# Performance work log

Hardware: AMD Instinct MI355X
Metric: run time of the kernel (lower is better)

Reference implementation:

```python
import jax, jax.numpy as jnp
import numpy as np

COMMIT = 0.5  # commitment from Discriminator init


def _sn(w):
    """Spectral norm, 1 power iteration from a deterministic start vector."""
    W = w.reshape(w.shape[0], -1)
    u = jnp.ones((W.shape[0],), w.dtype) / jnp.sqrt(jnp.asarray(W.shape[0], w.dtype))
    v = W.T @ u
    v = jax.lax.stop_gradient(v / (jnp.linalg.norm(v) + 1e-8))
    u2 = W @ v
    u2 = jax.lax.stop_gradient(u2 / (jnp.linalg.norm(u2) + 1e-8))
    sigma = u2 @ (W @ v)
    return w / sigma


def _conv(h, w, b, pad):
    y = jax.lax.conv_general_dilated(h, _sn(w), (1, 1), [(pad, pad), (pad, pad)],
                                     dimension_numbers=("NCHW", "OIHW", "NCHW"))
    return y + b[None, :, None, None]


def _pool(h):  # AvgPool2d(2)
    B, C, H, W = h.shape
    return h.reshape(B, C, H // 2, 2, W // 2, 2).mean(axis=(3, 5))


def _dblock(h, w1, b1, w2, b2, wsc, bsc, preact, down):
    y = jax.nn.relu(h) if preact else h
    y = _conv(y, w1, b1, 1)
    y = _conv(jax.nn.relu(y), w2, b2, 1)
    if down:
        y = _pool(y)
    sc = h
    if preact:
        if wsc is not None:
            sc = _conv(sc, wsc, bsc, 0)
        if down:
            sc = _pool(sc)
    else:
        if down:
            sc = _pool(sc)
        if wsc is not None:
            sc = _conv(sc, wsc, bsc, 0)
    return y + sc


def _quantize(h, embed):
    """VQ step (eval mode, no EMA). h: [B,C,H,W], embed: [C,K]."""
    B, C, H, W = h.shape
    xp = jnp.transpose(h, (0, 2, 3, 1))            # [B,H,W,C]
    flat = xp.reshape(-1, C)                       # [N,C]
    dist = (jnp.sum(flat ** 2, 1, keepdims=True)
            - 2.0 * flat @ embed
            + jnp.sum(embed ** 2, 0, keepdims=True))  # [N,K]
    ind = jnp.argmin(dist, axis=1)                 # [N]
    q = embed.T[ind].reshape(xp.shape)             # gather codebook rows
    diff = COMMIT * jnp.mean((jax.lax.stop_gradient(q) - xp) ** 2, axis=(1, 2, 3)).reshape(B, 1)
    q_st = xp + jax.lax.stop_gradient(q - xp)      # straight-through (unused downstream, as in source)
    K = embed.shape[1]
    probs = jnp.zeros((K,), flat.dtype).at[ind].add(1.0) / flat.shape[0]
    ppl = jnp.exp(-jnp.sum(probs * jnp.log(probs + 1e-10)))
    return jnp.transpose(q_st, (0, 3, 1, 2)), diff, ppl


def setup_inputs() -> dict:
    key = jax.random.key(0)
    ks = iter(jax.random.split(key, 40))
    d = {}
    d["x"] = jax.random.normal(next(ks), (64, 3, 32, 32), jnp.float32)
    d["y"] = jax.random.randint(next(ks), (64,), 0, 100)
    def w(shape):
        return 0.02 * jax.random.normal(next(ks), shape, jnp.float32)
    # block 0: 3->256, downsample, learnable sc
    d["b0_w1"] = w((256, 3, 3, 3));   d["b0_b1"] = jnp.zeros((256,), jnp.float32)
    d["b0_w2"] = w((256, 256, 3, 3)); d["b0_b2"] = jnp.zeros((256,), jnp.float32)
    d["b0_wsc"] = w((256, 3, 1, 1)); d["b0_bsc"] = jnp.zeros((256,), jnp.float32)
    # block 1: 256->256, downsample, learnable sc
    d["b1_w1"] = w((256, 256, 3, 3)); d["b1_b1"] = jnp.zeros((256,), jnp.float32)
    d["b1_w2"] = w((256, 256, 3, 3)); d["b1_b2"] = jnp.zeros((256,), jnp.float32)
    d["b1_wsc"] = w((256, 256, 1, 1)); d["b1_bsc"] = jnp.zeros((256,), jnp.float32)
    # blocks 2,3: 256->256, no downsample, identity sc
    d["b2_w1"] = w((256, 256, 3, 3)); d["b2_b1"] = jnp.zeros((256,), jnp.float32)
    d["b2_w2"] = w((256, 256, 3, 3)); d["b2_b2"] = jnp.zeros((256,), jnp.float32)
    d["b3_w1"] = w((256, 256, 3, 3)); d["b3_b1"] = jnp.zeros((256,), jnp.float32)
    d["b3_w2"] = w((256, 256, 3, 3)); d["b3_b2"] = jnp.zeros((256,), jnp.float32)
    # VQ codebooks: torch.randn(dim, n_embed)
    for i in range(4):
        d[f"cb{i}"] = jax.random.normal(next(ks), (256, 1024), jnp.float32)
    d["lin_w"] = w((1, 256)); d["lin_b"] = jnp.zeros((1,), jnp.float32)
    d["emb_w"] = w((100, 256))
    return d


def reference(x, y, b0_w1, b0_b1, b0_w2, b0_b2, b0_wsc, b0_bsc,
              b1_w1, b1_b1, b1_w2, b1_b2, b1_wsc, b1_bsc,
              b2_w1, b2_b1, b2_w2, b2_b2, b3_w1, b3_b1, b3_w2, b3_b2,
              cb0, cb1, cb2, cb3, lin_w, lin_b, emb_w):
    h = _dblock(x, b0_w1, b0_b1, b0_w2, b0_b2, b0_wsc, b0_bsc, preact=False, down=True)
    _, d0, _ = _quantize(h, cb0)   # quantized output discarded, as in source
    h = _dblock(h, b1_w1, b1_b1, b1_w2, b1_b2, b1_wsc, b1_bsc, preact=True, down=True)
    _, d1, _ = _quantize(h, cb1)
    h = _dblock(h, b2_w1, b2_b1, b2_w2, b2_b2, None, None, preact=True, down=False)
    _, d2, _ = _quantize(h, cb2)
    h = _dblock(h, b3_w1, b3_b1, b3_w2, b3_b2, None, None, preact=True, down=False)
    _, d3, ppl = _quantize(h, cb3)
    quant_loss = d0 + d1 + d2 + d3                 # [B,1]
    hf = jnp.sum(jax.nn.relu(h), axis=(2, 3))      # [B,256]
    out = hf @ _sn(lin_w).T + lin_b                # [B,1]
    out = out + jnp.sum(_sn(emb_w)[y] * hf, axis=1, keepdims=True)
    return (out, quant_loss, ppl)
```

## Files before the change

kernel.cpp:

```cpp
#include <hip/hip_runtime.h>
#include <math.h>

typedef __attribute__((ext_vector_type(8))) short s8v;
typedef __attribute__((ext_vector_type(4))) float f4v;

__device__ inline ushort f2bf(float x) {
    unsigned u = __float_as_uint(x);
    unsigned r = (u + 0x7FFFu + ((u >> 16) & 1u)) >> 16;
    return (ushort)r;
}
__device__ inline float bf2f(ushort h) { return __uint_as_float(((unsigned)h) << 16); }
__device__ inline float sig_of(double n2) { return (float)(n2 / (sqrt(n2) + 1e-8)); }

#define DEV __global__ __launch_bounds__(256)

struct SnMeta { const float* w[12]; int O[12]; int M[12]; };
struct SnRMap { short mat[85]; short row0[85]; };

DEV void snv2_kernel(SnMeta a, SnRMap mp, double* __restrict__ vbufraw) {
    int b = blockIdx.x;
    int id = mp.mat[b];
    int r0 = mp.row0[b];
    int O = a.O[id], M = a.M[id];
    int rend = min(r0 + 32, O);
    const float* W = a.w[id];
    for (int m = threadIdx.x; m < M; m += 256) {
        double s = 0.0;
        for (int o = r0; o < rend; ++o) s += (double)W[(size_t)o * M + m];
        atomicAdd(vbufraw + id * 2304 + m, s);
    }
}

DEV void snn_kernel(SnMeta a, const double* __restrict__ vbufraw, double* __restrict__ vnorm2) {
    int id = blockIdx.x;
    int M = a.M[id];
    double u0 = 1.0 / sqrt((double)a.O[id]);
    __shared__ double red[256];
    double ps = 0.0;
    for (int m = threadIdx.x; m < M; m += 256) { double v = vbufraw[id * 2304 + m] * u0; ps += v * v; }
    red[threadIdx.x] = ps; __syncthreads();
    for (int st = 128; st > 0; st >>= 1) { if (threadIdx.x < st) red[threadIdx.x] += red[threadIdx.x + st]; __syncthreads(); }
    if (threadIdx.x == 0) vnorm2[id] = red[0];
}

DEV void snu_kernel(SnMeta a, const double* __restrict__ vbufraw,
                    const double* __restrict__ vnorm2, double* __restrict__ unorm2) {
    int wv = blockIdx.x * 4 + (threadIdx.x >> 6);
    int lane = threadIdx.x & 63;
    const int cumR[13] = {0, 256, 512, 768, 1024, 1280, 1536, 1792, 2048, 2304, 2560, 2561, 2661};
    if (wv >= 2661) return;
    int id = 0;
    for (int i = 0; i < 12; ++i) if (wv >= cumR[i]) id = i;
    int o = wv - cumR[id];
    int M = a.M[id];
    double u0 = 1.0 / sqrt((double)a.O[id]);
    const float* Wr = a.w[id] + (size_t)o * M;
    const double* vb = vbufraw + id * 2304;
    double s = 0.0;
    for (int m = lane; m < M; m += 64) s += (double)Wr[m] * vb[m];
    for (int off = 32; off > 0; off >>= 1) s += __shfl_down(s, off, 64);
    if (lane == 0) {
        double s1 = 1.0 / (sqrt(vnorm2[id]) + 1e-8);
        double u = s * u0 * s1;
        atomicAdd(unorm2 + id, u * u);
    }
}

struct PrepArgs {
    const float* w[8]; int C[8]; int sigidx[8]; int outoff[8]; int nel[8];
    const float* cb[4];
};

DEV void prep_all_kernel(PrepArgs a, const double* __restrict__ unorm2,
                         ushort* __restrict__ wp, ushort* __restrict__ ep,
                         double* __restrict__ en64) {
    int blk = blockIdx.x;
    if (blk < 1824) {
        int gid = blk * 256 + threadIdx.x;
        int L = 0, cum = 0;
        for (int i = 0; i < 8; ++i) { int n9 = a.nel[i] / 9; if (gid >= cum && gid < cum + n9) { L = i; break; } cum += a.nel[i] / 9; }
        if (gid >= cum + a.nel[L] / 9) return;
        int e9 = gid - cum;
        if (L == 0) {
            int oc = e9 >> 5, k = e9 & 31;
            float inv = 1.f / sig_of(unorm2[0]);
            float v = 0.f;
            if (k < 27) v = a.w[0][((size_t)(oc * 3 + (k % 3))) * 9 + (k / 3)] * inv;
            ushort h = f2bf(v);
            ushort l = f2bf(v - bf2f(h));
            wp[oc * 32 + k] = h;
            wp[8192 + oc * 32 + k] = l;
            return;
        }
        int C = a.C[L];
        int NICC = (C + 31) >> 5;
        int icl = e9 & 31;
        int oc = (e9 >> 5) & 255;
        int icc = e9 >> 13;
        int ic = icc * 32 + icl;
        float inv = 1.f / sig_of(unorm2[a.sigidx[L]]);
        const float* wr = (ic < C) ? (a.w[L] + ((size_t)oc * C + ic) * 9) : nullptr;
        int nel = a.nel[L];
        int base = a.outoff[L] + icc * 8192 + oc * 32 + icl;
        #pragma unroll
        for (int tap = 0; tap < 9; ++tap) {
            float v = wr ? wr[tap] * inv : 0.f;
            ushort h = f2bf(v);
            ushort l = f2bf(v - bf2f(h));
            int o = base + tap * NICC * 8192;
            wp[o] = h;
            wp[o + nel] = l;
        }
    } else if (blk < 1824 + 4096) {
        int gid = (blk - 1824) * 256 + threadIdx.x;
        int layer = gid >> 18;
        int e = gid & 262143;
        int c5 = e & 31, k = (e >> 5) & 1023, icc = e >> 15;
        float v = a.cb[layer][(size_t)(icc * 32 + c5) * 1024 + k];
        ushort h = f2bf(v);
        ushort l = f2bf(v - bf2f(h));
        size_t o = (size_t)layer * 524288 + ((size_t)icc * 1024 + k) * 64 + c5;
        ep[o] = h; ep[o + 32] = l;
    } else {
        int b2 = blk - 1824 - 4096;
        int cc = b2 & 7, layer = b2 >> 3;
        const float* cb = a.cb[layer];
        int t = threadIdx.x;
        double d[4] = {};
        for (int c = cc * 32; c < cc * 32 + 32; ++c) {
            #pragma unroll
            for (int j = 0; j < 4; ++j) {
                double v = (double)cb[(size_t)c * 1024 + t + j * 256];
                d[j] += v * v;
            }
        }
        #pragma unroll
        for (int j = 0; j < 4; ++j) atomicAdd(en64 + layer * 1024 + t + j * 256, d[j]);
    }
}

DEV void enfin_kernel(const double* __restrict__ en64, float* __restrict__ en) {
    int gid = blockIdx.x * 256 + threadIdx.x;
    en[gid] = (float)en64[gid];
}

__global__ __launch_bounds__(256) void conv01k_kernel(
        const float* __restrict__ x, const ushort* __restrict__ wp0,
        const float* __restrict__ bias, ushort* __restrict__ outs) {
    __shared__ float sX[3][10][10];
    __shared__ ushort sI[64][72];
    int t = threadIdx.x, wid = t >> 6, lane = t & 63, quad = lane >> 4, l15 = lane & 15;
    int n = blockIdx.z;
    int tIdx = blockIdx.x;
    int th0 = (tIdx >> 2) * 8, tw0 = (tIdx & 3) * 8;
    for (int i = t; i < 300; i += 256) {
        int ch = i / 100, r = i - (i / 100) * 100;
        int yy = r / 10, xx = r - (r / 10) * 10;
        int gy = th0 - 1 + yy, gx = tw0 - 1 + xx;
        float v = 0.f;
        if (gy >= 0 && gy < 32 && gx >= 0 && gx < 32) v = x[(((size_t)n * 3 + ch) * 32 + gy) * 32 + gx];
        sX[ch][yy][xx] = v;
    }
    __syncthreads();
    for (int i = t; i < 2048; i += 256) {
        int px = i >> 5, k = i & 31;
        float v = 0.f;
        if (k < 27) {
            int tap = k / 3, ch = k - tap * 3;
            int ty = tap / 3, tx = tap - ty * 3;
            v = sX[ch][(px >> 3) + ty][(px & 7) + tx];
        }
        ushort hv = f2bf(v);
        sI[px][k] = hv;
        sI[px][32 + k] = f2bf(v - bf2f(hv));
    }
    __syncthreads();
    int ocb = wid * 64;
    f4v acc[4][4];
    #pragma unroll
    for (int mt = 0; mt < 4; ++mt)
        #pragma unroll
        for (int nt = 0; nt < 4; ++nt) acc[mt][nt] = (f4v){0.f, 0.f, 0.f, 0.f};
    s8v ah[4], al[4], bh[4], bl[4];
    #pragma unroll
    for (int mt = 0; mt < 4; ++mt) {
        ah[mt] = *(const s8v*)&sI[mt * 16 + l15][quad * 8];
        al[mt] = *(const s8v*)&sI[mt * 16 + l15][32 + quad * 8];
    }
    #pragma unroll
    for (int nt = 0; nt < 4; ++nt) {
        int oc = ocb + nt * 16 + l15;
        bh[nt] = *(const s8v*)(wp0 + oc * 32 + quad * 8);
        bl[nt] = *(const s8v*)(wp0 + 8192 + oc * 32 + quad * 8);
    }
    #pragma unroll
    for (int mt = 0; mt < 4; ++mt)
        #pragma unroll
        for (int nt = 0; nt < 4; ++nt) {
            acc[mt][nt] = __builtin_amdgcn_mfma_f32_16x16x32_bf16(al[mt], bh[nt], acc[mt][nt], 0, 0, 0);
            acc[mt][nt] = __builtin_amdgcn_mfma_f32_16x16x32_bf16(ah[mt], bl[nt], acc[mt][nt], 0, 0, 0);
            acc[mt][nt] = __builtin_amdgcn_mfma_f32_16x16x32_bf16(ah[mt], bh[nt], acc[mt][nt], 0, 0, 0);
        }
    #pragma unroll
    for (int nt = 0; nt < 4; ++nt) {
        int oc = ocb + nt * 16 + l15;
        float bv = bias[oc];
        int iccg = oc >> 5, ocw = oc & 31;
        #pragma unroll
        for (int mt = 0; mt < 4; ++mt) {
            #pragma unroll
            for (int r = 0; r < 4; ++r) {
                int px = mt * 16 + quad * 4 + r;
                int y = th0 + (px >> 3), xx = tw0 + (px & 7);
                float v = fmaxf(acc[mt][nt][r] + bv, 0.f);
                ushort h = f2bf(v);
                size_t ob = ((((size_t)n * 32 + y) * 32 + xx) * 8 + iccg) * 64;
                outs[ob + ocw] = h;
                outs[ob + 32 + ocw] = f2bf(v - bf2f(h));
            }
        }
    }
}

template<int PX>
DEV void vq2_kernel(const float* __restrict__ h, const float* __restrict__ cb,
                    const ushort* __restrict__ ep, const float* __restrict__ en,
                    float* __restrict__ dacc, int* __restrict__ hist,
                    ushort* __restrict__ hs, int HW) {
    const int MT = PX / 16;
    const int SUBS = 256 / PX;
    __shared__ ushort sA[8 * PX * 66];
    __shared__ unsigned long long sKey[PX][65];
    __shared__ int sKst[PX];
    __shared__ float sPart[PX][SUBS];
    __shared__ double sSum[PX];
    int t = threadIdx.x, wid = t >> 6, lane = t & 63, quad = lane >> 4, l15 = lane & 15;
    int pix0 = blockIdx.x * PX, n = pix0 / HW, s0 = pix0 % HW;
    const float* hb = h + (size_t)n * 256 * HW + s0;

    for (int i = t; i < 256 * PX; i += 256) {
        int c = i / PX, p = i % PX;
        float v = hb[(size_t)c * HW + p];
        ushort hv = f2bf(v), lv = f2bf(v - bf2f(hv));
        int a = (c >> 5) * (PX * 66) + p * 66 + (c & 31);
        sA[a] = hv; sA[a + 32] = lv;
    }
    __syncthreads();

    if (hs) {
        for (int i = t; i < PX * 32; i += 256) {
            int p = i >> 5; int rem = i & 31; int icc = rem >> 2, q = rem & 3;
            int aoff = icc * (PX * 66) + p * 66 + q * 8;
            s8v hv = *(const s8v*)&sA[aoff];
            s8v lv = *(const s8v*)&sA[aoff + 32];
            #pragma unroll
            for (int j = 0; j < 8; ++j) {
                float f = bf2f((ushort)hv[j]) + bf2f((ushort)lv[j]);
                if (f <= 0.f) { hv[j] = 0; lv[j] = 0; }
            }
            size_t ob = (((size_t)n * HW + s0 + p) * 8 + icc) * 64 + q * 8;
            *(s8v*)(hs + ob) = hv;
            *(s8v*)(hs + ob + 32) = lv;
        }
    }

    unsigned long long best[MT][4];
    #pragma unroll
    for (int mt = 0; mt < MT; ++mt)
        #pragma unroll
        for (int r = 0; r < 4; ++r) best[mt][r] = ~0ull;

    for (int kp = 0; kp < 2; ++kp) {
        f4v acc[MT][8];
        #pragma unroll
        for (int mt = 0; mt < MT; ++mt)
            #pragma unroll
            for (int nt = 0; nt < 8; ++nt) acc[mt][nt] = (f4v){0.f, 0.f, 0.f, 0.f};
        for (int icc = 0; icc < 8; ++icc) {
            #pragma unroll
            for (int ntc = 0; ntc < 2; ++ntc) {
                s8v eh[4], el[4];
                #pragma unroll
                for (int j = 0; j < 4; ++j) {
                    int k = wid * 256 + kp * 128 + (ntc * 4 + j) * 16 + l15;
                    const ushort* q = ep + ((size_t)icc * 1024 + k) * 64 + quad * 8;
                    eh[j] = *(const s8v*)q; el[j] = *(const s8v*)(q + 32);
                }
                #pragma unroll
                for (int mt = 0; mt < MT; ++mt) {
                    int a = icc * (PX * 66) + (mt * 16 + l15) * 66 + quad * 8;
                    s8v ah = *(const s8v*)&sA[a], al = *(const s8v*)&sA[a + 32];
                    #pragma unroll
                    for (int j = 0; j < 4; ++j) {
                        int nt = ntc * 4 + j;
                        acc[mt][nt] = __builtin_amdgcn_mfma_f32_16x16x32_bf16(al, eh[j], acc[mt][nt], 0, 0, 0);
                        acc[mt][nt] = __builtin_amdgcn_mfma_f32_16x16x32_bf16(ah, el[j], acc[mt][nt], 0, 0, 0);
                        acc[mt][nt] = __builtin_amdgcn_mfma_f32_16x16x32_bf16(ah, eh[j], acc[mt][nt], 0, 0, 0);
                    }
                }
            }
        }
        #pragma unroll
        for (int mt = 0; mt < MT; ++mt)
            #pragma unroll
            for (int nt = 0; nt < 8; ++nt) {
                int k = wid * 256 + kp * 128 + nt * 16 + l15;
                float ev = en[k];
                #pragma unroll
                for (int r = 0; r < 4; ++r) {
                    float s = ev - 2.f * acc[mt][nt][r];
                    unsigned ub = __float_as_uint(s);
                    ub = ((int)ub < 0) ? ~ub : (ub | 0x80000000u);
                    unsigned long long key = ((unsigned long long)ub << 32) | (unsigned)k;
                    if (key < best[mt][r]) best[mt][r] = key;
                }
            }
    }
    #pragma unroll
    for (int mt = 0; mt < MT; ++mt)
        #pragma unroll
        for (int r = 0; r < 4; ++r) {
            int p = mt * 16 + quad * 4 + r;
            sKey[p][wid * 16 + l15] = best[mt][r];
        }
    __syncthreads();
    if (t < PX) {
        unsigned long long m = ~0ull;
        for (int j = 0; j < 64; ++j) { unsigned long long v = sKey[t][j]; if (v < m) m = v; }
        sKst[t] = (int)(unsigned)(m & 0xFFFFFFFFu);
    }
    __syncthreads();
    {
        int p = t % PX, sub = t / PX;
        int ks = sKst[p];
        const float* ec = cb + ks;
        float d = 0.f;
        for (int c = sub * PX; c < sub * PX + PX; ++c) {
            float xv = hb[(size_t)c * HW + p];
            float evv = ec[(size_t)c * 1024];
            float df = xv - evv;
            d += df * df;
        }
        sPart[p][sub] = d;
    }
    __syncthreads();
    if (t < PX) {
        float s = 0.f;
        for (int j = 0; j < SUBS; ++j) s += sPart[t][j];
        sSum[t] = (double)s;
        if (hist) atomicAdd(hist + sKst[t], 1);
    }
    __syncthreads();
    if (t == 0) {
        double s = 0.0;
        for (int i = 0; i < PX; ++i) s += sSum[i];
        atomicAdd(dacc + n, (float)s);
    }
}

template<int ST, int NW, int NTW, int NICC, bool RELU, bool POOL, bool RES, bool INS, bool OUTS, bool SC0>
__global__ __launch_bounds__(NW * 64) void conv_mfma(
        const float* __restrict__ in, const ushort* __restrict__ ins,
        const ushort* __restrict__ wp, const float* __restrict__ bias,
        const float* __restrict__ res, float* __restrict__ out,
        ushort* __restrict__ outs, int C, int H,
        const float* __restrict__ scw, const float* __restrict__ scb,
        const double* __restrict__ un2) {
    const int MT = ST * 4;
    const int PLANE = NICC * 73728;
    const int SASZ = ST * 100 * 72;
    const int NITER = (ST * 100 * 8 + NW * 64 - 1) / (NW * 64);
    __shared__ ushort sA[(INS ? 2 : 1) * SASZ];
    __shared__ float sSC[3][16];
    int t = threadIdx.x;
    int wid = t >> 6, lane = t & 63, quad = lane >> 4, l15 = lane & 15;
    int n = blockIdx.z;
    int ocb = blockIdx.y * (NW * NTW * 16) + wid * (NTW * 16);
    int tpr = H >> 3;
    int tIdx0 = blockIdx.x * ST;

    int abase[MT];
    #pragma unroll
    for (int mt = 0; mt < MT; ++mt) {
        int m64 = (mt & 3) * 16 + l15;
        abase[mt] = (((mt >> 2) * 100 + (m64 >> 3) * 10 + (m64 & 7)) * 72) + quad * 8;
    }

    unsigned gofs[INS ? NITER : 1];
    s8v pref[INS ? NITER : 1];
    if (INS) {
        #pragma unroll
        for (int it = 0; it < NITER; ++it) {
            int i = t + it * NW * 64;
            gofs[it] = 0xFFFFFFFFu;
            if (i < ST * 100 * 8) {
                int pg = i >> 3, part = i & 7;
                int tile = pg / 100, pos = pg - tile * 100;
                int tIdx = tIdx0 + tile;
                int th0 = (tIdx / tpr) * 8, tw0 = (tIdx % tpr) * 8;
                int gy = th0 - 1 + pos / 10, gx = tw0 - 1 + (pos % 10);
                if (gy >= 0 && gy < H && gx >= 0 && gx < H)
                    gofs[it] = (unsigned)((((n * H + gy) * H + gx) * 8) * 64 + part * 8);
            }
        }
        #pragma unroll
        for (int it = 0; it < NITER; ++it)
            pref[it] = (gofs[it] != 0xFFFFFFFFu) ? *(const s8v*)(ins + gofs[it])
                                                 : (s8v){0, 0, 0, 0, 0, 0, 0, 0};
        #pragma unroll
        for (int it = 0; it < NITER; ++it) {
            int i = t + it * NW * 64;
            if (i < ST * 100 * 8) *(s8v*)(&sA[(i >> 3) * 72 + (i & 7) * 8]) = pref[it];
        }
        if (NICC > 1) {
            #pragma unroll
            for (int it = 0; it < NITER; ++it)
                pref[it] = (gofs[it] != 0xFFFFFFFFu) ? *(const s8v*)(ins + gofs[it] + 64)
                                                     : (s8v){0, 0, 0, 0, 0, 0, 0, 0};
        }
        __syncthreads();
    }

    f4v acc[MT][NTW];
    #pragma unroll
    for (int mt = 0; mt < MT; ++mt)
        #pragma unroll
        for (int nt = 0; nt < NTW; ++nt)
            acc[mt][nt] = (f4v){0.f, 0.f, 0.f, 0.f};

    for (int icc = 0; icc < NICC; ++icc) {
        int bufbase = INS ? (icc & 1) * SASZ : 0;
        if (INS) {
            if (icc + 1 < NICC) {
                int nb = ((icc + 1) & 1) * SASZ;
                #pragma unroll
                for (int it = 0; it < NITER; ++it) {
                    int i = t + it * NW * 64;
                    if (i < ST * 100 * 8) *(s8v*)(&sA[nb + (i >> 3) * 72 + (i & 7) * 8]) = pref[it];
                }
                if (icc + 2 < NICC) {
                    #pragma unroll
                    for (int it = 0; it < NITER; ++it)
                        pref[it] = (gofs[it] != 0xFFFFFFFFu) ? *(const s8v*)(ins + gofs[it] + (unsigned)(icc + 2) * 64)
                                                             : (s8v){0, 0, 0, 0, 0, 0, 0, 0};
                }
            }
        } else {
            __syncthreads();
            for (int i = t; i < ST * 100 * 32; i += NW * 64) {
                int ic = i / (ST * 100);
                int rr = i - ic * (ST * 100);
                int tile = rr / 100, pos = rr - (rr / 100) * 100;
                int tIdx = tIdx0 + tile;
                int th0 = (tIdx / tpr) * 8, tw0 = (tIdx % tpr) * 8;
                int gy = th0 - 1 + pos / 10, gx = tw0 - 1 + (pos % 10);
                int gic = icc * 32 + ic;
                ushort hv = 0, lv = 0;
                if (gic < C && gy >= 0 && gy < H && gx >= 0 && gx < H) {
                    float v = in[(((size_t)n * C + gic) * H + gy) * H + gx];
                    if (RELU) v = fmaxf(v, 0.f);
                    hv = f2bf(v);
                    lv = f2bf(v - bf2f(hv));
                }
                int si = (tile * 100 + pos) * 72 + ic;
                sA[si] = hv; sA[si + 32] = lv;
            }
            __syncthreads();
        }

        s8v bh[2][NTW], bl[2][NTW];
        {
            size_t wb = (size_t)icc * 8192;
            #pragma unroll
            for (int nt = 0; nt < NTW; ++nt) {
                size_t wo = wb + (size_t)(ocb + nt * 16 + l15) * 32 + quad * 8;
                bh[0][nt] = *(const s8v*)(wp + wo);
                bl[0][nt] = *(const s8v*)(wp + PLANE + wo);
            }
        }
        #pragma unroll
        for (int tap = 0; tap < 9; ++tap) {
            int cb = tap & 1;
            if (tap < 8) {
                size_t wb = (size_t)((tap + 1) * NICC + icc) * 8192;
                #pragma unroll
                for (int nt = 0; nt < NTW; ++nt) {
                    size_t wo = wb + (size_t)(ocb + nt * 16 + l15) * 32 + quad * 8;
                    bh[cb ^ 1][nt] = *(const s8v*)(wp + wo);
                    bl[cb ^ 1][nt] = *(const s8v*)(wp + PLANE + wo);
                }
            }
            int toff = ((tap / 3) * 10 + (tap % 3)) * 72;
            #pragma unroll
            for (int mt = 0; mt < MT; ++mt) {
                s8v ah = *(const s8v*)(&sA[bufbase + abase[mt] + toff]);
                s8v al = *(const s8v*)(&sA[bufbase + abase[mt] + toff + 32]);
                #pragma unroll
                for (int nt = 0; nt < NTW; ++nt) {
                    acc[mt][nt] = __builtin_amdgcn_mfma_f32_16x16x32_bf16(al, bh[cb][nt], acc[mt][nt], 0, 0, 0);
                    acc[mt][nt] = __builtin_amdgcn_mfma_f32_16x16x32_bf16(ah, bl[cb][nt], acc[mt][nt], 0, 0, 0);
                    acc[mt][nt] = __builtin_amdgcn_mfma_f32_16x16x32_bf16(ah, bh[cb][nt], acc[mt][nt], 0, 0, 0);
                }
            }
        }
        if (INS && icc + 1 < NICC) __syncthreads();
    }

    if (SC0) {
        __syncthreads();
        if (t < 48) {
            int ic = t >> 4, p = t & 15;
            int py = p >> 2, px = p & 3;
            int th0 = (tIdx0 / tpr) * 8, tw0 = (tIdx0 % tpr) * 8;
            const float* xb = in + (((size_t)(n * 3 + ic)) * 32 + th0 + 2 * py) * 32 + tw0 + 2 * px;
            sSC[ic][p] = 0.25f * (xb[0] + xb[1] + xb[32] + xb[33]);
        }
        __syncthreads();
    }

    #pragma unroll
    for (int nt = 0; nt < NTW; ++nt) {
        int oc = ocb + nt * 16 + l15;
        float bv = bias[oc];
        #pragma unroll
        for (int mt = 0; mt < MT; ++mt) {
            int tIdx = tIdx0 + (mt >> 2);
            int th0 = (tIdx / tpr) * 8, tw0 = (tIdx % tpr) * 8;
            if (POOL) {
                float s01 = acc[mt][nt][0] + acc[mt][nt][1];
                float s23 = acc[mt][nt][2] + acc[mt][nt][3];
                float o01 = s01 + __shfl_down(s01, 32, 64);
                float o23 = s23 + __shfl_down(s23, 32, 64);
                if (quad < 2) {
                    int Ho = H >> 1;
                    int oy = (th0 >> 1) + (mt & 3);
                    int ox = (tw0 >> 1) + quad * 2;
                    size_t ob = ((size_t)(n * 256 + oc) * Ho + oy) * Ho;
                    float v0 = 0.25f * o01 + bv;
                    float v1 = 0.25f * o23 + bv;
                    if (SC0) {
                        int p0 = (mt & 3) * 4 + quad * 2;
                        float scale = 1.f / sig_of(un2[2]);
                        float sa0 = scb[oc], sa1 = scb[oc];
                        #pragma unroll
                        for (int ic = 0; ic < 3; ++ic) {
                            float wv = scw[oc * 3 + ic] * scale;
                            sa0 += sSC[ic][p0] * wv;
                            sa1 += sSC[ic][p0 + 1] * wv;
                        }
                        v0 += sa0;
                        v1 += sa1;
                    }
                    out[ob + ox] = v0;
                    out[ob + ox + 1] = v1;
                }
            } else if (OUTS) {
                int iccg = oc >> 5, ocw = oc & 31;
                #pragma unroll
                for (int r = 0; r < 4; ++r) {
                    int p16 = quad * 4 + r;
                    int y = th0 + (mt & 3) * 2 + (p16 >> 3);
                    int x = tw0 + (p16 & 7);
                    float v = fmaxf(acc[mt][nt][r] + bv, 0.f);
                    ushort h = f2bf(v);
                    size_t ob = ((((size_t)n * H + y) * H + x) * 8 + iccg) * 64;
                    outs[ob + ocw] = h;
                    outs[ob + 32 + ocw] = f2bf(v - bf2f(h));
                }
            } else {
                #pragma unroll
                for (int r = 0; r < 4; ++r) {
                    int p16 = quad * 4 + r;
                    int y = th0 + (mt & 3) * 2 + (p16 >> 3);
                    int x = tw0 + (p16 & 7);
                    size_t oi = (((size_t)(n * 256 + oc)) * H + y) * H + x;
                    float v = acc[mt][nt][r] + bv;
                    if (RES) v += res[oi];
                    out[oi] = v;
                }
            }
        }
    }
}

DEV void sc1_kernel(const float* __restrict__ h1, const float* __restrict__ wsc,
                    const float* __restrict__ bsc, const double* __restrict__ unorm2,
                    float* __restrict__ h2) {
    __shared__ float sP[64][64];
    __shared__ float sWs[64][65];
    int t = threadIdx.x;
    int n = blockIdx.x, ocb = blockIdx.y * 64;
    int ocg = t & 15, pgr = t >> 4;
    float scale = 1.f / sig_of(unorm2[5]);
    float acc[4][4] = {};
    for (int c0 = 0; c0 < 256; c0 += 64) {
        __syncthreads();
        for (int i = t; i < 4096; i += 256) {
            int ic = i >> 6, p = i & 63;
            int oh = p >> 3, ow = p & 7;
            const float* hb = h1 + (((size_t)(n * 256 + c0 + ic)) * 16 + oh * 2) * 16 + ow * 2;
            sP[ic][p] = 0.25f * (hb[0] + hb[1] + hb[16] + hb[17]);
            int oc = i >> 6, ic2 = i & 63;
            sWs[oc][ic2] = wsc[(size_t)(ocb + oc) * 256 + c0 + ic2] * scale;
        }
        __syncthreads();
        for (int ic = 0; ic < 64; ++ic) {
            float pv[4];
            #pragma unroll
            for (int q = 0; q < 4; ++q) pv[q] = sP[ic][pgr * 4 + q];
            #pragma unroll
            for (int j = 0; j < 4; ++j) {
                float wv = sWs[ocg + 16 * j][ic];
                #pragma unroll
                for (int q = 0; q < 4; ++q) acc[j][q] += wv * pv[q];
            }
        }
    }
    #pragma unroll
    for (int j = 0; j < 4; ++j) {
        int oc = ocb + ocg + 16 * j;
        float bv = bsc[oc];
        #pragma unroll
        for (int q = 0; q < 4; ++q) {
            size_t oi = ((size_t)(n * 256 + oc)) * 64 + pgr * 4 + q;
            h2[oi] += acc[j][q] + bv;
        }
    }
}

DEV void headppl_kernel(const float* __restrict__ h4, const float* __restrict__ lin_w,
                        const float* __restrict__ lin_b, const float* __restrict__ emb_w,
                        const int* __restrict__ y, const double* __restrict__ unorm2,
                        const float* __restrict__ dacc, const int* __restrict__ hist,
                        float* __restrict__ out) {
    __shared__ double r1[256], r2[256];
    int b = blockIdx.x, t = threadIdx.x;
    const float* hb = h4 + ((size_t)b * 256 + t) * 64;
    float s = 0.f;
    #pragma unroll 4
    for (int i = 0; i < 64; ++i) s += fmaxf(hb[i], 0.f);
    int yb = y[b];
    r1[t] = (double)s * (double)lin_w[t];
    r2[t] = (double)s * (double)emb_w[(size_t)yb * 256 + t];
    __syncthreads();
    for (int st = 128; st > 0; st >>= 1) { if (t < st) { r1[t] += r1[t + st]; r2[t] += r2[t + st]; } __syncthreads(); }
    if (t == 0) {
        out[b] = (float)(r1[0] / (double)sig_of(unorm2[10]) + (double)lin_b[0] + r2[0] / (double)sig_of(unorm2[11]));
        out[64 + b] = (float)(0.5 * ((double)dacc[b] * (1.0 / 65536.0)
                              + ((double)dacc[64 + b] + (double)dacc[128 + b] + (double)dacc[192 + b]) * (1.0 / 16384.0)));
    }
    if (b == 0) {
        __syncthreads();
        double ps = 0.0;
        for (int k = t; k < 1024; k += 256) {
            double p = (double)hist[k] * (1.0 / 4096.0);
            ps += p * log(p + 1e-10);
        }
        r1[t] = ps; __syncthreads();
        for (int st = 128; st > 0; st >>= 1) { if (t < st) r1[t] += r1[t + st]; __syncthreads(); }
        if (t == 0) out[128] = (float)exp(-r1[0]);
    }
}

extern "C" void kernel_launch(void* const* d_in, const int* in_sizes, int n_in,
                              void* d_out, int out_size, void* d_ws, size_t ws_size,
                              hipStream_t stream) {
    (void)in_sizes; (void)n_in; (void)out_size; (void)ws_size;
    const float* x      = (const float*)d_in[0];
    const int*   y      = (const int*)  d_in[1];
    const float* b0_w1  = (const float*)d_in[2];
    const float* b0_b1  = (const float*)d_in[3];
    const float* b0_w2  = (const float*)d_in[4];
    const float* b0_b2  = (const float*)d_in[5];
    const float* b0_wsc = (const float*)d_in[6];
    const float* b0_bsc = (const float*)d_in[7];
    const float* b1_w1  = (const float*)d_in[8];
    const float* b1_b1  = (const float*)d_in[9];
    const float* b1_w2  = (const float*)d_in[10];
    const float* b1_b2  = (const float*)d_in[11];
    const float* b1_wsc = (const float*)d_in[12];
    const float* b1_bsc = (const float*)d_in[13];
    const float* b2_w1  = (const float*)d_in[14];
    const float* b2_b1  = (const float*)d_in[15];
    const float* b2_w2  = (const float*)d_in[16];
    const float* b2_b2  = (const float*)d_in[17];
    const float* b3_w1  = (const float*)d_in[18];
    const float* b3_b1  = (const float*)d_in[19];
    const float* b3_w2  = (const float*)d_in[20];
    const float* b3_b2  = (const float*)d_in[21];
    const float* cb0    = (const float*)d_in[22];
    const float* cb1    = (const float*)d_in[23];
    const float* cb2    = (const float*)d_in[24];
    const float* cb3    = (const float*)d_in[25];
    const float* lin_w  = (const float*)d_in[26];
    const float* lin_b  = (const float*)d_in[27];
    const float* emb_w  = (const float*)d_in[28];
    float* out = (float*)d_out;

    float* wsf  = (float*)d_ws;
    float* dacc = wsf + 16;
    double* vnorm2 = (double*)(wsf + 512);
    double* unorm2 = (double*)(wsf + 544);
    int*   hist = (int*)(wsf + 1296);
    double* en64 = (double*)(wsf + 2560);
    float* en   = wsf + 10752;
    ushort* Aus  = (ushort*)(wsf + 65536);
    ushort* tbus = (ushort*)(wsf + 65536);
    ushort* t2us = (ushort*)(wsf + 4259840);
    ushort* h1s  = (ushort*)(wsf + 5308416);
    ushort* h2s  = (ushort*)(wsf + 9502720);
    ushort* h3s  = (ushort*)(wsf + 10551296);
    float* h1 = wsf + 16842752;
    float* h2 = h1 + 4194304;
    float* h3 = h2 + 1048576;
    float* h4 = h3 + 1048576;
    ushort* wp = (ushort*)(wsf + 24182784);
    double* vbufraw = (double*)(wsf + 28385280);
    ushort* ep = (ushort*)(wsf + 28440576);

    hipMemsetAsync(wsf, 0, 10752 * sizeof(float), stream);
    hipMemsetAsync(vbufraw, 0, 27648 * sizeof(double), stream);

    SnMeta sm;
    const float* sw[12] = {b0_w1, b0_w2, b0_wsc, b1_w1, b1_w2, b1_wsc,
                           b2_w1, b2_w2, b3_w1, b3_w2, lin_w, emb_w};
    int sO[12] = {256, 256, 256, 256, 256, 256, 256, 256, 256, 256, 1, 100};
    int sM[12] = {27, 2304, 3, 2304, 2304, 256, 2304, 2304, 2304, 2304, 256, 256};
    for (int i = 0; i < 12; ++i) { sm.w[i] = sw[i]; sm.O[i] = sO[i]; sm.M[i] = sM[i]; }
    SnRMap rp;
    {
        int bi = 0;
        for (int i = 0; i < 12; ++i) {
            int nb = (sO[i] + 31) / 32;
            for (int j = 0; j < nb; ++j) { rp.mat[bi] = (short)i; rp.row0[bi] = (short)(j * 32); ++bi; }
        }
    }
    snv2_kernel<<<85, 256, 0, stream>>>(sm, rp, vbufraw);
    snn_kernel<<<12, 256, 0, stream>>>(sm, vbufraw, vnorm2);
    snu_kernel<<<666, 256, 0, stream>>>(sm, vbufraw, vnorm2, unorm2);

    PrepArgs pa;
    const float* pw[8] = {b0_w1, b0_w2, b1_w1, b1_w2, b2_w1, b2_w2, b3_w1, b3_w2};
    int pC[8]   = {3, 256, 256, 256, 256, 256, 256, 256};
    int pS[8]   = {0, 1, 3, 4, 6, 7, 8, 9};
    int pOff[8] = {0, 147456, 1327104, 2506752, 3686400, 4866048, 6045696, 7225344};
    int pN[8]   = {73728, 589824, 589824, 589824, 589824, 589824, 589824, 589824};
    for (int i = 0; i < 8; ++i) { pa.w[i] = pw[i]; pa.C[i] = pC[i]; pa.sigidx[i] = pS[i]; pa.outoff[i] = pOff[i]; pa.nel[i] = pN[i]; }
    pa.cb[0] = cb0; pa.cb[1] = cb1; pa.cb[2] = cb2; pa.cb[3] = cb3;
    prep_all_kernel<<<5952, 256, 0, stream>>>(pa, unorm2, wp, ep, en64);
    enfin_kernel<<<16, 256, 0, stream>>>(en64, en);

    conv01k_kernel<<<dim3(16, 1, 64), 256, 0, stream>>>(x, wp, b0_b1, Aus);
    conv_mfma<1, 4, 2, 8, false, true, false, true, false, true><<<dim3(16, 2, 64), 256, 0, stream>>>(
        x, Aus, wp + 147456, b0_b2, nullptr, h1, nullptr, 256, 32, b0_wsc, b0_bsc, unorm2);
    vq2_kernel<32><<<512, 256, 0, stream>>>(h1, cb0, ep + 0, en + 0, dacc + 0, nullptr, h1s, 256);

    conv_mfma<1, 4, 1, 8, false, false, false, true, true, false><<<dim3(4, 4, 64), 256, 0, stream>>>(
        nullptr, h1s, wp + 1327104, b1_b1, nullptr, nullptr, tbus, 256, 16, nullptr, nullptr, nullptr);
    conv_mfma<1, 4, 1, 8, false, true, false, true, false, false><<<dim3(4, 4, 64), 256, 0, stream>>>(
        nullptr, tbus, wp + 2506752, b1_b2, nullptr, h2, nullptr, 256, 16, nullptr, nullptr, nullptr);
    sc1_kernel<<<dim3(64, 4), 256, 0, stream>>>(h1, b1_wsc, b1_bsc, unorm2, h2);
    vq2_kernel<16><<<256, 256, 0, stream>>>(h2, cb1, ep + 524288, en + 1024, dacc + 64, nullptr, h2s, 64);

    conv_mfma<1, 2, 1, 8, false, false, false, true, true, false><<<dim3(1, 8, 64), 128, 0, stream>>>(
        nullptr, h2s, wp + 3686400, b2_b1, nullptr, nullptr, t2us, 256, 8, nullptr, nullptr, nullptr);
    conv_mfma<1, 2, 1, 8, false, false, true, true, false, false><<<dim3(1, 8, 64), 128, 0, stream>>>(
        nullptr, t2us, wp + 4866048, b2_b2, h2, h3, nullptr, 256, 8, nullptr, nullptr, nullptr);
    vq2_kernel<16><<<256, 256, 0, stream>>>(h3, cb2, ep + 1048576, en + 2048, dacc + 128, nullptr, h3s, 64);

    conv_mfma<1, 2, 1, 8, false, false, false, true, true, false><<<dim3(1, 8, 64), 128, 0, stream>>>(
        nullptr, h3s, wp + 6045696, b3_b1, nullptr, nullptr, t2us, 256, 8, nullptr, nullptr, nullptr);
    conv_mfma<1, 2, 1, 8, false, false, true, true, false, false><<<dim3(1, 8, 64), 128, 0, stream>>>(
        nullptr, t2us, wp + 7225344, b3_b2, h3, h4, nullptr, 256, 8, nullptr, nullptr, nullptr);
    vq2_kernel<16><<<256, 256, 0, stream>>>(h4, cb3, ep + 1572864, en + 3072, dacc + 192, hist, nullptr, 64);

    headppl_kernel<<<64, 256, 0, stream>>>(h4, lin_w, lin_b, emb_w, y, unorm2, dacc, hist, out);
}
```

Before: 1.040 ms.

## Store block0 output as packed split-bf16 and drop codebook-norm finalize kernel

Block 0's conv now writes its pooled output directly in the split hi/lo bf16 channel-grouped layout. The VQ0 kernel and the shortcut kernel read that layout instead of the fp32 NCHW tensor, which removes the per-element conversion and the strided fp32 loads. Codebook norms are accumulated with float atomics straight into the final buffer, which eliminates the enfin kernel launch. In exchange, the norm sums lose double-precision accumulation across atomics, and the VQ distance uses reconstructed hi+lo values.

```diff
diff --git a/kernel.cpp b/kernel.cpp
--- a/kernel.cpp
+++ b/kernel.cpp
@@ -73,7 +73,7 @@
 
 DEV void prep_all_kernel(PrepArgs a, const double* __restrict__ unorm2,
                          ushort* __restrict__ wp, ushort* __restrict__ ep,
-                         double* __restrict__ en64) {
+                         float* __restrict__ en) {
     int blk = blockIdx.x;
     if (blk < 1824) {
         int gid = blk * 256 + threadIdx.x;
@@ -135,13 +135,8 @@
             }
         }
         #pragma unroll
-        for (int j = 0; j < 4; ++j) atomicAdd(en64 + layer * 1024 + t + j * 256, d[j]);
-    }
-}
-
-DEV void enfin_kernel(const double* __restrict__ en64, float* __restrict__ en) {
-    int gid = blockIdx.x * 256 + threadIdx.x;
-    en[gid] = (float)en64[gid];
+        for (int j = 0; j < 4; ++j) atomicAdd(en + layer * 1024 + t + j * 256, (float)d[j]);
+    }
 }
 
 __global__ __launch_bounds__(256) void conv01k_kernel(
@@ -223,7 +218,8 @@
 }
 
 template<int PX>
-DEV void vq2_kernel(const float* __restrict__ h, const float* __restrict__ cb,
+DEV void vq2_kernel(const float* __restrict__ h, const ushort* __restrict__ hps,
+                    const float* __restrict__ cb,
                     const ushort* __restrict__ ep, const float* __restrict__ en,
                     float* __restrict__ dacc, int* __restrict__ hist,
                     ushort* __restrict__ hs, int HW) {
@@ -236,14 +232,22 @@
     __shared__ double sSum[PX];
     int t = threadIdx.x, wid = t >> 6, lane = t & 63, quad = lane >> 4, l15 = lane & 15;
     int pix0 = blockIdx.x * PX, n = pix0 / HW, s0 = pix0 % HW;
-    const float* hb = h + (size_t)n * 256 * HW + s0;
-
-    for (int i = t; i < 256 * PX; i += 256) {
-        int c = i / PX, p = i % PX;
-        float v = hb[(size_t)c * HW + p];
-        ushort hv = f2bf(v), lv = f2bf(v - bf2f(hv));
-        int a = (c >> 5) * (PX * 66) + p * 66 + (c & 31);
-        sA[a] = hv; sA[a + 32] = lv;
+    const float* hb = h ? (h + (size_t)n * 256 * HW + s0) : nullptr;
+
+    if (hps) {
+        for (int i = t; i < PX * 64; i += 256) {
+            int p = i >> 6, rem = i & 63, icc = rem >> 3, part = rem & 7;
+            size_t src = ((size_t)(n * HW + s0 + p) * 8 + icc) * 64 + part * 8;
+            *(s8v*)&sA[icc * (PX * 66) + p * 66 + part * 8] = *(const s8v*)(hps + src);
+        }
+    } else {
+        for (int i = t; i < 256 * PX; i += 256) {
+            int c = i / PX, p = i % PX;
+            float v = hb[(size_t)c * HW + p];
+            ushort hv = f2bf(v), lv = f2bf(v - bf2f(hv));
+            int a = (c >> 5) * (PX * 66) + p * 66 + (c & 31);
+            sA[a] = hv; sA[a + 32] = lv;
+        }
     }
     __syncthreads();
 
@@ -336,7 +340,13 @@
         const float* ec = cb + ks;
         float d = 0.f;
         for (int c = sub * PX; c < sub * PX + PX; ++c) {
-            float xv = hb[(size_t)c * HW + p];
+            float xv;
+            if (hps) {
+                int a = (c >> 5) * (PX * 66) + p * 66 + (c & 31);
+                xv = bf2f(sA[a]) + bf2f(sA[a + 32]);
+            } else {
+                xv = hb[(size_t)c * HW + p];
+            }
             float evv = ec[(size_t)c * 1024];
             float df = xv - evv;
             d += df * df;
@@ -535,7 +545,6 @@
                     int Ho = H >> 1;
                     int oy = (th0 >> 1) + (mt & 3);
                     int ox = (tw0 >> 1) + quad * 2;
-                    size_t ob = ((size_t)(n * 256 + oc) * Ho + oy) * Ho;
                     float v0 = 0.25f * o01 + bv;
                     float v1 = 0.25f * o23 + bv;
                     if (SC0) {
@@ -551,8 +560,20 @@
                         v0 += sa0;
                         v1 += sa1;
                     }
-                    out[ob + ox] = v0;
-                    out[ob + ox + 1] = v1;
+                    if (OUTS) {
+                        int iccg = oc >> 5, ocw = oc & 31;
+                        size_t ob0 = ((((size_t)n * Ho + oy) * Ho + ox) * 8 + iccg) * 64;
+                        size_t ob1 = ((((size_t)n * Ho + oy) * Ho + ox + 1) * 8 + iccg) * 64;
+                        ushort h0 = f2bf(v0), h1v = f2bf(v1);
+                        outs[ob0 + ocw] = h0;
+                        outs[ob0 + 32 + ocw] = f2bf(v0 - bf2f(h0));
+                        outs[ob1 + ocw] = h1v;
+                        outs[ob1 + 32 + ocw] = f2bf(v1 - bf2f(h1v));
+                    } else {
+                        size_t ob = ((size_t)(n * 256 + oc) * Ho + oy) * Ho;
+                        out[ob + ox] = v0;
+                        out[ob + ox + 1] = v1;
+                    }
                 }
             } else if (OUTS) {
                 int iccg = oc >> 5, ocw = oc & 31;
@@ -583,7 +604,7 @@
     }
 }
 
-DEV void sc1_kernel(const float* __restrict__ h1, const float* __restrict__ wsc,
+DEV void sc1_kernel(const ushort* __restrict__ h1ps, const float* __restrict__ wsc,
                     const float* __restrict__ bsc, const double* __restrict__ unorm2,
                     float* __restrict__ h2) {
     __shared__ float sP[64][64];
@@ -598,8 +619,18 @@
         for (int i = t; i < 4096; i += 256) {
             int ic = i >> 6, p = i & 63;
             int oh = p >> 3, ow = p & 7;
-            const float* hb = h1 + (((size_t)(n * 256 + c0 + ic)) * 16 + oh * 2) * 16 + ow * 2;
-            sP[ic][p] = 0.25f * (hb[0] + hb[1] + hb[16] + hb[17]);
+            int cch = c0 + ic;
+            int cg = (cch >> 5) * 64 + (cch & 31);
+            float s = 0.f;
+            #pragma unroll
+            for (int dy = 0; dy < 2; ++dy)
+                #pragma unroll
+                for (int dx = 0; dx < 2; ++dx) {
+                    int pix = (oh * 2 + dy) * 16 + ow * 2 + dx;
+                    size_t a = ((size_t)(n * 256 + pix)) * 512 + cg;
+                    s += bf2f(h1ps[a]) + bf2f(h1ps[a + 32]);
+                }
+            sP[ic][p] = 0.25f * s;
             int oc = i >> 6, ic2 = i & 63;
             sWs[oc][ic2] = wsc[(size_t)(ocb + oc) * 256 + c0 + ic2] * scale;
         }
@@ -702,7 +733,6 @@
     double* vnorm2 = (double*)(wsf + 512);
     double* unorm2 = (double*)(wsf + 544);
     int*   hist = (int*)(wsf + 1296);
-    double* en64 = (double*)(wsf + 2560);
     float* en   = wsf + 10752;
     ushort* Aus  = (ushort*)(wsf + 65536);
     ushort* tbus = (ushort*)(wsf + 65536);
@@ -710,15 +740,15 @@
     ushort* h1s  = (ushort*)(wsf + 5308416);
     ushort* h2s  = (ushort*)(wsf + 9502720);
     ushort* h3s  = (ushort*)(wsf + 10551296);
-    float* h1 = wsf + 16842752;
-    float* h2 = h1 + 4194304;
+    ushort* h1ps = (ushort*)(wsf + 16842752);
+    float* h2 = wsf + 21037056;
     float* h3 = h2 + 1048576;
     float* h4 = h3 + 1048576;
     ushort* wp = (ushort*)(wsf + 24182784);
     double* vbufraw = (double*)(wsf + 28385280);
     ushort* ep = (ushort*)(wsf + 28440576);
 
-    hipMemsetAsync(wsf, 0, 10752 * sizeof(float), stream);
+    hipMemsetAsync(wsf, 0, 14848 * sizeof(float), stream);
     hipMemsetAsync(vbufraw, 0, 27648 * sizeof(double), stream);
 
     SnMeta sm;
@@ -747,32 +777,31 @@
     int pN[8]   = {73728, 589824, 589824, 589824, 589824, 589824, 589824, 589824};
     for (int i = 0; i < 8; ++i) { pa.w[i] = pw[i]; pa.C[i] = pC[i]; pa.sigidx[i] = pS[i]; pa.outoff[i] = pOff[i]; pa.nel[i] = pN[i]; }
     pa.cb[0] = cb0; pa.cb[1] = cb1; pa.cb[2] = cb2; pa.cb[3] = cb3;
-    prep_all_kernel<<<5952, 256, 0, stream>>>(pa, unorm2, wp, ep, en64);
-    enfin_kernel<<<16, 256, 0, stream>>>(en64, en);
+    prep_all_kernel<<<5952, 256, 0, stream>>>(pa, unorm2, wp, ep, en);
 
     conv01k_kernel<<<dim3(16, 1, 64), 256, 0, stream>>>(x, wp, b0_b1, Aus);
-    conv_mfma<1, 4, 2, 8, false, true, false, true, false, true><<<dim3(16, 2, 64), 256, 0, stream>>>(
-        x, Aus, wp + 147456, b0_b2, nullptr, h1, nullptr, 256, 32, b0_wsc, b0_bsc, unorm2);
-    vq2_kernel<32><<<512, 256, 0, stream>>>(h1, cb0, ep + 0, en + 0, dacc + 0, nullptr, h1s, 256);
+    conv_mfma<1, 4, 2, 8, false, true, false, true, true, true><<<dim3(16, 2, 64), 256, 0, stream>>>(
+        x, Aus, wp + 147456, b0_b2, nullptr, nullptr, h1ps, 256, 32, b0_wsc, b0_bsc, unorm2);
+    vq2_kernel<32><<<512, 256, 0, stream>>>(nullptr, h1ps, cb0, ep + 0, en + 0, dacc + 0, nullptr, h1s, 256);
 
     conv_mfma<1, 4, 1, 8, false, false, false, true, true, false><<<dim3(4, 4, 64), 256, 0, stream>>>(
         nullptr, h1s, wp + 1327104, b1_b1, nullptr, nullptr, tbus, 256, 16, nullptr, nullptr, nullptr);
     conv_mfma<1, 4, 1, 8, false, true, false, true, false, false><<<dim3(4, 4, 64), 256, 0, stream>>>(
         nullptr, tbus, wp + 2506752, b1_b2, nullptr, h2, nullptr, 256, 16, nullptr, nullptr, nullptr);
-    sc1_kernel<<<dim3(64, 4), 256, 0, stream>>>(h1, b1_wsc, b1_bsc, unorm2, h2);
-    vq2_kernel<16><<<256, 256, 0, stream>>>(h2, cb1, ep + 524288, en + 1024, dacc + 64, nullptr, h2s, 64);
+    sc1_kernel<<<dim3(64, 4), 256, 0, stream>>>(h1ps, b1_wsc, b1_bsc, unorm2, h2);
+    vq2_kernel<16><<<256, 256, 0, stream>>>(h2, nullptr, cb1, ep + 524288, en + 1024, dacc + 64, nullptr, h2s, 64);
 
     conv_mfma<1, 2, 1, 8, false, false, false, true, true, false><<<dim3(1, 8, 64), 128, 0, stream>>>(
         nullptr, h2s, wp + 3686400, b2_b1, nullptr, nullptr, t2us, 256, 8, nullptr, nullptr, nullptr);
     conv_mfma<1, 2, 1, 8, false, false, true, true, false, false><<<dim3(1, 8, 64), 128, 0, stream>>>(
         nullptr, t2us, wp + 4866048, b2_b2, h2, h3, nullptr, 256, 8, nullptr, nullptr, nullptr);
-    vq2_kernel<16><<<256, 256, 0, stream>>>(h3, cb2, ep + 1048576, en + 2048, dacc + 128, nullptr, h3s, 64);
+    vq2_kernel<16><<<256, 256, 0, stream>>>(h3, nullptr, cb2, ep + 1048576, en + 2048, dacc + 128, nullptr, h3s, 64);
 
     conv_mfma<1, 2, 1, 8, false, false, false, true, true, false><<<dim3(1, 8, 64), 128, 0, stream>>>(
         nullptr, h3s, wp + 6045696, b3_b1, nullptr, nullptr, t2us, 256, 8, nullptr, nullptr, nullptr);
     conv_mfma<1, 2, 1, 8, false, false, true, true, false, false><<<dim3(1, 8, 64), 128, 0, stream>>>(
         nullptr, t2us, wp + 7225344, b3_b2, h3, h4, nullptr, 256, 8, nullptr, nullptr, nullptr);
-    vq2_kernel<16><<<256, 256, 0, stream>>>(h4, cb3, ep + 1572864, en + 3072, dacc + 192, hist, nullptr, 64);
+    vq2_kernel<16><<<256, 256, 0, stream>>>(h4, nullptr, cb3, ep + 1572864, en + 3072, dacc + 192, hist, nullptr, 64);
 
     headppl_kernel<<<64, 256, 0, stream>>>(h4, lin_w, lin_b, emb_w, y, unorm2, dacc, hist, out);
 }
```

Measured after the change: 1.063 ms. +2.2%, slower.
